# Kernel optimization log

Measured on AMD Instinct MI355X. Metric: run time of the kernel, lower is better.

The kernel has to match this reference:

```python
import jax, jax.numpy as jnp
import numpy as np

EPS = 1e-8


def _conv1d(x, w, b):
    # x: [B, E, L], w: [F, E, K], b: [F] -> [B, F, L] (k=3, pad=1 keeps length)
    y = jax.lax.conv_general_dilated(
        x, w, window_strides=(1,), padding=[(1, 1)],
        dimension_numbers=("NCH", "OIH", "NCH"))
    return y + b[None, :, None]


def setup_inputs() -> dict:
    key = jax.random.key(0)
    kq, ka, ke, kw, kb, ku = jax.random.split(key, 6)
    B, QL, AL = 512, 128, 512
    V, E, F, K = 50000, 300, 400, 3
    question = jax.random.randint(kq, (B, QL), 0, V + 1, dtype=jnp.int64)
    answer = jax.random.randint(ka, (B, AL), 0, V + 1, dtype=jnp.int64)
    emb_table = jax.random.normal(ke, (V + 1, E), dtype=jnp.float32)
    emb_table = emb_table.at[0].set(0.0)  # padding_idx=0
    conv_w = jax.random.normal(kw, (F, E, K), dtype=jnp.float32) * 0.05
    conv_b = jax.random.normal(kb, (F,), dtype=jnp.float32) * 0.05
    U = jax.random.normal(ku, (F, F), dtype=jnp.float32) * 0.1
    return {"question": question, "answer": answer, "emb_table": emb_table,
            "conv_w": conv_w, "conv_b": conv_b, "U": U}


def reference(question, answer, emb_table, conv_w, conv_b, U):
    q = emb_table[question]              # [B, QL, E]
    a = emb_table[answer]                # [B, AL, E]
    Q = _conv1d(q.transpose(0, 2, 1), conv_w, conv_b)   # [B, F, QL]
    A = _conv1d(a.transpose(0, 2, 1), conv_w, conv_b)   # [B, F, AL]
    # G = tanh(Q^T U A): [B, QL, AL]
    G = jnp.tanh(jnp.einsum("bfq,fg,bga->bqa", Q, U, A))
    roQ = jax.nn.softmax(jnp.max(G, axis=2), axis=1)    # [B, QL]
    roA = jax.nn.softmax(jnp.max(G, axis=1), axis=1)    # [B, AL]
    rQ = jnp.einsum("bfq,bq->bf", Q, roQ)               # [B, F]
    rA = jnp.einsum("bfa,ba->bf", A, roA)               # [B, F]
    nQ = jnp.maximum(jnp.linalg.norm(rQ, axis=1), EPS)
    nA = jnp.maximum(jnp.linalg.norm(rA, axis=1), EPS)
    return jnp.sum(rQ * rA, axis=1) / (nQ * nA)         # [B]
```

## Files before the change

### kernel.cpp

```cpp
#include <hip/hip_runtime.h>
#include <math.h>

typedef unsigned int   uint32;
typedef unsigned short ushort16;
typedef __attribute__((ext_vector_type(8))) short  short8;
typedef __attribute__((ext_vector_type(4))) float  floatx4;

#define Bb   512
#define QLn  128
#define ALn  512
#define En   300
#define Fn   400
#define OW   416
#define EPAD 320
#define NV   50001
#define ECROWS 50176
#define ECSTRIDE 2560

typedef const __attribute__((address_space(1))) unsigned int guint_t;
typedef __attribute__((address_space(3))) unsigned int luint_t;
#define GLDS16(g, l) __builtin_amdgcn_global_load_lds((guint_t*)(g), (luint_t*)(l), 16, 0, 0)

static __device__ __forceinline__ float bf_lo(uint32 u) { return __uint_as_float(u << 16); }
static __device__ __forceinline__ float bf_hi(uint32 u) { return __uint_as_float(u & 0xffff0000u); }
static __device__ __forceinline__ ushort16 f2bf(float f) {
    uint32 u = __float_as_uint(f);
    uint32 r = (u + 0x7fffu + ((u >> 16) & 1u)) >> 16;
    return (ushort16)r;
}
static __device__ __forceinline__ uint32 pack2(float a, float b) {
    return (uint32)f2bf(a) | ((uint32)f2bf(b) << 16);
}

__global__ __launch_bounds__(128) void embcvt_kernel(
        const float* __restrict__ emb, char* __restrict__ embbf)
{
    const int r = blockIdx.x, j = threadIdx.x;
    const float* er = emb + (size_t)r * En;
    uint32* orow = (uint32*)(embbf + (size_t)r * 640);
    for (int d = j; d < 160; d += 128) {
        uint32 v = 0;
        if (d < 150) {
            float2 f2v = *(const float2*)(er + 2 * d);
            v = pack2(f2v.x, f2v.y);
        }
        orow[d] = v;
    }
}

__global__ __launch_bounds__(256) void prep_wt(
        const float* __restrict__ W, const float* __restrict__ cb,
        ushort16* __restrict__ Wt2, float* __restrict__ bias2)
{
    const int f = blockIdx.x, t = threadIdx.x;
    for (int p2 = t; p2 < 480; p2 += 256) {
        int p = 2 * p2;
        float v0 = 0.f, v1 = 0.f;
        if (f < Fn) {
            int kk = p / EPAD, e = p - kk * EPAD;
            if (e < En)     v0 = W[(size_t)f * 900 + e * 3 + kk];
            if (e + 1 < En) v1 = W[(size_t)f * 900 + (e + 1) * 3 + kk];
        }
        *(uint32*)&Wt2[(size_t)f * 960 + p] = pack2(v0, v1);
    }
    if (t == 0) bias2[f] = (f < Fn) ? cb[f] : 0.f;
}

__global__ __launch_bounds__(256) void prep_ub(
        const float* __restrict__ U, ushort16* __restrict__ Ub)
{
    const int g = blockIdx.x, t = threadIdx.x;
    uint32* orow = (uint32*)(Ub + (size_t)g * 416);
    for (int f2 = t; f2 < 208; f2 += 256) {
        int f = 2 * f2;
        float v0 = 0.f, v1 = 0.f;
        if (g < Fn) {
            if (f < Fn)     v0 = U[(size_t)f * Fn + g];
            if (f + 1 < Fn) v1 = U[(size_t)(f + 1) * Fn + g];
        }
        orow[f2] = pack2(v0, v1);
    }
}

__global__ __launch_bounds__(512) void ec_gemm(
        const char* __restrict__ embbf, const char* __restrict__ Wt2,
        char* __restrict__ EC)
{
    __shared__ __align__(16) char As[32768];
    __shared__ __align__(16) char Bs[32768];
    const int t = threadIdx.x, lane = t & 63, w = t >> 6;
    const int v0 = blockIdx.x * 256, c0 = blockIdx.y * 256;
    const int wr = w >> 2, wc = w & 3;
    const int fm = lane & 15;
    const int cg = ((lane & 3) - ((lane >> 3) & 3)) & 3;
    const int rl = lane >> 2;
    const int chunkOff = (((lane >> 4) + (fm >> 1)) & 3) * 16;

    const char* srcA[2];
    const char* srcB[2];
#pragma unroll
    for (int i = 0; i < 2; ++i) {
        srcA[i] = embbf + (size_t)(v0 + w * 32 + i * 16 + rl) * 640 + cg * 16;
        int n = c0 + w * 32 + i * 16 + rl;
        int kk = n / 416, f = n - kk * 416;
        if (n >= 1248) { kk = 0; f = 508; }
        srcB[i] = Wt2 + (size_t)f * 1920 + kk * 640 + cg * 16;
    }
    char* AsW = As + w * 2048;
    char* BsW = Bs + w * 2048;

    floatx4 acc[8][4];
    const floatx4 zz = {0.f, 0.f, 0.f, 0.f};
#pragma unroll
    for (int m = 0; m < 8; ++m)
#pragma unroll
        for (int n = 0; n < 4; ++n) acc[m][n] = zz;

#define ESTG(ko, buf) do {                                                    \
        const int _ko = (ko); const int _bo = (buf) * 16384;                  \
        GLDS16(srcA[0] + _ko, AsW + _bo);                                     \
        GLDS16(srcA[1] + _ko, AsW + _bo + 1024);                              \
        GLDS16(srcB[0] + _ko, BsW + _bo);                                     \
        GLDS16(srcB[1] + _ko, BsW + _bo + 1024);                              \
    } while (0)

    int cur = 0;
    ESTG(0, 0);
    __syncthreads();
    for (int ks = 0; ks < 10; ++ks) {
        const int nxt = cur ^ 1;
        if (ks < 9) ESTG((ks + 1) * 64, nxt);
        short8 af[8], bfv[4];
        const char* Ac = As + cur * 16384;
        const char* Bc = Bs + cur * 16384;
#pragma unroll
        for (int m = 0; m < 8; ++m)
            af[m] = *(const short8*)(Ac + (wr * 128 + m * 16 + fm) * 64 + chunkOff);
#pragma unroll
        for (int n = 0; n < 4; ++n)
            bfv[n] = *(const short8*)(Bc + (wc * 64 + n * 16 + fm) * 64 + chunkOff);
        __builtin_amdgcn_s_setprio(1);
#pragma unroll
        for (int m = 0; m < 8; ++m)
#pragma unroll
            for (int n = 0; n < 4; ++n)
                acc[m][n] = __builtin_amdgcn_mfma_f32_16x16x32_bf16(
                    af[m], bfv[n], acc[m][n], 0, 0, 0);
        __builtin_amdgcn_s_setprio(0);
        __syncthreads();
        cur = nxt;
    }
#undef ESTG

#pragma unroll
    for (int m = 0; m < 8; ++m) {
        const int v = v0 + wr * 128 + m * 16 + ((lane >> 4) * 4);
#pragma unroll
        for (int n = 0; n < 4; ++n) {
            const int col = c0 + wc * 64 + n * 16 + fm;
#pragma unroll
            for (int r = 0; r < 4; ++r)
                *(ushort16*)(EC + (size_t)(v + r) * ECSTRIDE + col * 2) =
                    f2bf(acc[m][n][r]);
        }
    }
}

static __device__ __forceinline__ void gather_one(
        const int* __restrict__ toks, const char* __restrict__ EC,
        const float* __restrict__ bias2, char* __restrict__ outb,
        int id, int L)
{
    const uint32 uid = (uint32)id;
    const int c = (int)(uid % 52u);
    const int r = (int)(uid / 52u);
    const int l = r & (L - 1), b = r / L;
    const int* tr = toks + (size_t)b * L;
    const int t0 = (l > 0)     ? tr[l - 1] : 0;
    const int t1 = tr[l];
    const int t2 = (l < L - 1) ? tr[l + 1] : 0;
    const uint4 x0 = *(const uint4*)(EC + (size_t)t0 * ECSTRIDE +        c * 16);
    const uint4 x1 = *(const uint4*)(EC + (size_t)t1 * ECSTRIDE +  832 + c * 16);
    const uint4 x2 = *(const uint4*)(EC + (size_t)t2 * ECSTRIDE + 1664 + c * 16);
    const float4 b0 = *(const float4*)(bias2 + c * 8);
    const float4 b1 = *(const float4*)(bias2 + c * 8 + 4);
    uint4 o;
    o.x = pack2(bf_lo(x0.x) + bf_lo(x1.x) + bf_lo(x2.x) + b0.x,
                bf_hi(x0.x) + bf_hi(x1.x) + bf_hi(x2.x) + b0.y);
    o.y = pack2(bf_lo(x0.y) + bf_lo(x1.y) + bf_lo(x2.y) + b0.z,
                bf_hi(x0.y) + bf_hi(x1.y) + bf_hi(x2.y) + b0.w);
    o.z = pack2(bf_lo(x0.z) + bf_lo(x1.z) + bf_lo(x2.z) + b1.x,
                bf_hi(x0.z) + bf_hi(x1.z) + bf_hi(x2.z) + b1.y);
    o.w = pack2(bf_lo(x0.w) + bf_lo(x1.w) + bf_lo(x2.w) + b1.z,
                bf_hi(x0.w) + bf_hi(x1.w) + bf_hi(x2.w) + b1.w);
    *(uint4*)(outb + (size_t)r * 832 + c * 16) = o;
}

static __device__ __forceinline__ float red_sum_256(float v, volatile float* red) {
    int t = threadIdx.x;
    red[t] = v; __syncthreads();
    for (int s = 128; s > 0; s >>= 1) {
        if (t < s) red[t] = red[t] + red[t + s];
        __syncthreads();
    }
    float r = red[0]; __syncthreads();
    return r;
}

static __device__ __forceinline__ void pool_b_body(
        const float* __restrict__ scratch, float* __restrict__ out,
        int b, volatile float* red)
{
    const int t = threadIdx.x;
    float dd = 0.f, qq = 0.f, aam = 0.f;
    if (t < 208) {
        float q0 = 0.f, q1 = 0.f, a0 = 0.f, a1 = 0.f;
#pragma unroll
        for (int qtr = 0; qtr < 4; ++qtr) {
            const float* sc = scratch + ((size_t)b * 4 + qtr) * 832;
            q0 += sc[t]; q1 += sc[208 + t];
            a0 += sc[416 + t]; a1 += sc[624 + t];
        }
        dd  = q0 * a0 + q1 * a1;
        qq  = q0 * q0 + q1 * q1;
        aam = a0 * a0 + a1 * a1;
    }
    dd  = red_sum_256(dd, red);
    qq  = red_sum_256(qq, red);
    aam = red_sum_256(aam, red);
    if (t == 0) {
        float nq = fmaxf(sqrtf(qq), 1e-8f);
        float na = fmaxf(sqrtf(aam), 1e-8f);
        out[b] = dd / (nq * na);
    }
}

#define GQB 1024
#define GAB 4096
__global__ __launch_bounds__(256) void gather_both(
        const int* __restrict__ question, const int* __restrict__ answer,
        const char* __restrict__ EC, const float* __restrict__ bias2,
        char* __restrict__ qb, char* __restrict__ ab, int nb,
        const float* __restrict__ scrPrev, float* __restrict__ outPrev,
        int nbPrev)
{
    __shared__ float red[256];
    const int bx = blockIdx.x, t = threadIdx.x;
    if (bx < GQB) {
        const int total = nb * QLn * 52;
        for (int id = bx * 256 + t; id < total; id += GQB * 256)
            gather_one(question, EC, bias2, qb, id, QLn);
    } else if (bx < GQB + GAB) {
        const int total = nb * ALn * 52;
        for (int id = (bx - GQB) * 256 + t; id < total; id += GAB * 256)
            gather_one(answer, EC, bias2, ab, id, ALn);
    } else {
        const int b = bx - GQB - GAB;
        if (b < nbPrev) pool_b_body(scrPrev, outPrev, b, red);
    }
}

template<int MF, int NF, int BR>
static __device__ __forceinline__ void qp_tile64(
        const char* __restrict__ Qb, const char* __restrict__ Ub,
        char* __restrict__ ob, int col0, char* As, char* Bs)
{
    const int t = threadIdx.x, lane = t & 63, w = t >> 6;
    const int NWN = (MF == 4) ? 4 : 2;
    const int wr = w / NWN, wc = w % NWN;
    const int fm = lane & 15;
    const int cg = ((lane & 3) - ((lane >> 3) & 3)) & 3;
    const int rl = lane >> 2;
    const int chunkOff = (((lane >> 4) + (fm >> 1)) & 3) * 16;
    const int BUFB = BR * 64;

    const char* srcQ = Qb + (size_t)(w * 16 + rl) * 832 + cg * 16;
    const char* srcB0;
    const char* srcB1 = 0;
    if (BR == 256) {
        srcB0 = Ub + (size_t)(col0 + w * 64 + rl) * 832 + cg * 16;
    } else {
        srcB0 = Ub + (size_t)(col0 + w * 32 + rl) * 832 + cg * 16;
        srcB1 = Ub + (size_t)(col0 + 128 + w * 16 + rl) * 832 + cg * 16;
    }

    floatx4 acc[MF][NF];
    const floatx4 zz = {0.f, 0.f, 0.f, 0.f};
#pragma unroll
    for (int m = 0; m < MF; ++m)
#pragma unroll
        for (int n = 0; n < NF; ++n) acc[m][n] = zz;

#define QSTG(ko, buf) do {                                                    \
        const int _ko = (ko);                                                 \
        GLDS16(srcQ + _ko, As + (buf) * 4096 + w * 1024);                     \
        if (BR == 256) {                                                      \
            GLDS16(srcB0 + _ko,         Bs + (buf) * BUFB + w * 4096);        \
            GLDS16(srcB0 + 13312 + _ko, Bs + (buf) * BUFB + w * 4096 + 1024); \
            GLDS16(srcB0 + 26624 + _ko, Bs + (buf) * BUFB + w * 4096 + 2048); \
            GLDS16(srcB0 + 39936 + _ko, Bs + (buf) * BUFB + w * 4096 + 3072); \
        } else {                                                              \
            GLDS16(srcB0 + _ko,         Bs + (buf) * BUFB + w * 2048);        \
            GLDS16(srcB0 + 13312 + _ko, Bs + (buf) * BUFB + w * 2048 + 1024); \
            if (w < 2) GLDS16(srcB1 + _ko, Bs + (buf) * BUFB + 8192 + w * 1024); \
        }                                                                     \
    } while (0)

    int cur = 0;
    QSTG(0, 0);
    __syncthreads();
    for (int ks = 0; ks < 13; ++ks) {
        const int nxt = cur ^ 1;
        if (ks < 12) QSTG((ks + 1) * 64, nxt);
        short8 af[MF], bfv[NF];
        const char* Ac = As + cur * 4096;
        const char* Bc = Bs + cur * BUFB;
#pragma unroll
        for (int m = 0; m < MF; ++m)
            af[m] = *(const short8*)(Ac + (wr * (MF * 16) + m * 16 + fm) * 64 + chunkOff);
#pragma unroll
        for (int n = 0; n < NF; ++n)
            bfv[n] = *(const short8*)(Bc + (wc * (NF * 16) + n * 16 + fm) * 64 + chunkOff);
        __builtin_amdgcn_s_setprio(1);
#pragma unroll
        for (int m = 0; m < MF; ++m)
#pragma unroll
            for (int n = 0; n < NF; ++n)
                acc[m][n] = __builtin_amdgcn_mfma_f32_16x16x32_bf16(
                    af[m], bfv[n], acc[m][n], 0, 0, 0);
        __builtin_amdgcn_s_setprio(0);
        __syncthreads();
        cur = nxt;
    }
#undef QSTG

#pragma unroll
    for (int m = 0; m < MF; ++m) {
        const int row = wr * (MF * 16) + m * 16 + ((lane >> 4) * 4);
#pragma unroll
        for (int n = 0; n < NF; ++n) {
            const int col = col0 + wc * (NF * 16) + n * 16 + fm;
#pragma unroll
            for (int r = 0; r < 4; ++r)
                *(ushort16*)(ob + (size_t)(row + r) * 832 + col * 2) =
                    f2bf(acc[m][n][r]);
        }
    }
}

__global__ __launch_bounds__(256) void qp_gemm(
        const char* __restrict__ qb, const char* __restrict__ Ub,
        char* __restrict__ qpb, int nb)
{
    __shared__ __align__(16) char As[8192];
    __shared__ __align__(16) char Bs[32768];
    const int bx = blockIdx.x;
    const int xcd = bx & 7, rest = bx >> 3;
    const int nt = rest & 1, mh = (rest >> 1) & 1, b = (rest >> 2) * 8 + xcd;
    if (b >= nb) return;
    const char* Qb = qb + (size_t)b * 106496 + (size_t)mh * 64 * 832;
    char* ob = qpb + (size_t)b * 106496 + (size_t)mh * 64 * 832;
    if (nt == 0)
        qp_tile64<4, 4, 256>(Qb, Ub, ob, 0, As, Bs);
    else
        qp_tile64<2, 5, 160>(Qb, Ub, ob, 256, As, Bs);
}

__global__ __launch_bounds__(256) void fused_g(
        const ushort16* __restrict__ Qp,
        const ushort16* __restrict__ Av,
        float* __restrict__ rowPart,
        float* __restrict__ colMg,
        int nb)
{
    __shared__ __align__(16) char Qs[8192];
    __shared__ __align__(16) char Asl[32768];
    __shared__ float rowM4[64][4];

    const int t = threadIdx.x, lane = t & 63, w = t >> 6;
    const int bx = blockIdx.x;
    const int xcd = bx & 7, rest = bx >> 3;
    const int c = rest & 1, mh = (rest >> 1) & 1, b = (rest >> 2) * 8 + xcd;
    if (b >= nb) return;
    const int fm = lane & 15;
    const int cg = ((lane & 3) - ((lane >> 3) & 3)) & 3;
    const int rl = lane >> 2;
    const int chunkOff = (((lane >> 4) + (fm >> 1)) & 3) * 16;

    const char* Qpb = (const char*)Qp + (size_t)b * 106496 + (size_t)mh * 64 * 832;
    const char* Ab  = (const char*)Av + (size_t)b * 425984 + (size_t)c * 212992;
    const char* srcQ  = Qpb + (size_t)(w * 16 + rl) * 832 + cg * 16;
    const char* srcA0 = Ab  + (size_t)(w * 64 + rl) * 832 + cg * 16;

    floatx4 acc[4][4];
    const floatx4 zz = {0.f, 0.f, 0.f, 0.f};
#pragma unroll
    for (int m = 0; m < 4; ++m)
#pragma unroll
        for (int n = 0; n < 4; ++n) acc[m][n] = zz;

#define FSTG(ko, buf) do {                                                    \
        const int _ko = (ko);                                                 \
        GLDS16(srcQ + _ko,          Qs  + (buf) * 4096  + w * 1024);          \
        GLDS16(srcA0 + _ko,         Asl + (buf) * 16384 + w * 4096);          \
        GLDS16(srcA0 + 13312 + _ko, Asl + (buf) * 16384 + w * 4096 + 1024);   \
        GLDS16(srcA0 + 26624 + _ko, Asl + (buf) * 16384 + w * 4096 + 2048);   \
        GLDS16(srcA0 + 39936 + _ko, Asl + (buf) * 16384 + w * 4096 + 3072);   \
    } while (0)

    int cur = 0;
    FSTG(0, 0);
    __syncthreads();

    for (int ks = 0; ks < 13; ++ks) {
        const int nxt = cur ^ 1;
        if (ks < 12) FSTG((ks + 1) * 64, nxt);

        short8 qa[4], aa_[4];
        const char* Qc = Qs + cur * 4096;
        const char* Ac = Asl + cur * 16384;
#pragma unroll
        for (int m = 0; m < 4; ++m)
            qa[m] = *(const short8*)(Qc + (m * 16 + fm) * 64 + chunkOff);
#pragma unroll
        for (int n = 0; n < 4; ++n)
            aa_[n] = *(const short8*)(Ac + (w * 64 + n * 16 + fm) * 64 + chunkOff);
        __builtin_amdgcn_s_setprio(1);
#pragma unroll
        for (int m = 0; m < 4; ++m)
#pragma unroll
            for (int n = 0; n < 4; ++n)
                acc[m][n] = __builtin_amdgcn_mfma_f32_16x16x32_bf16(
                    qa[m], aa_[n], acc[m][n], 0, 0, 0);
        __builtin_amdgcn_s_setprio(0);
        __syncthreads();
        cur = nxt;
    }
#undef FSTG

#pragma unroll
    for (int m = 0; m < 4; ++m)
#pragma unroll
        for (int r = 0; r < 4; ++r) {
            float v = fmaxf(fmaxf(acc[m][0][r], acc[m][1][r]),
                            fmaxf(acc[m][2][r], acc[m][3][r]));
            v = fmaxf(v, __shfl_xor(v, 1));
            v = fmaxf(v, __shfl_xor(v, 2));
            v = fmaxf(v, __shfl_xor(v, 4));
            v = fmaxf(v, __shfl_xor(v, 8));
            if (fm == 0) rowM4[m * 16 + (lane >> 4) * 4 + r][w] = v;
        }
#pragma unroll
    for (int n = 0; n < 4; ++n) {
        float v = -1e30f;
#pragma unroll
        for (int m = 0; m < 4; ++m)
#pragma unroll
            for (int r = 0; r < 4; ++r) v = fmaxf(v, acc[m][n][r]);
        v = fmaxf(v, __shfl_xor(v, 16));
        v = fmaxf(v, __shfl_xor(v, 32));
        if (lane < 16)
            colMg[((size_t)b * 2 + mh) * 512 + c * 256 + w * 64 + n * 16 + lane] = v;
    }
    __syncthreads();
    if (t < 64)
        rowPart[((size_t)b * 2 + c) * 128 + mh * 64 + t] =
            fmaxf(fmaxf(rowM4[t][0], rowM4[t][1]),
                  fmaxf(rowM4[t][2], rowM4[t][3]));
}

static __device__ __forceinline__ float red_max_512(float v, volatile float* red) {
    int t = threadIdx.x;
    red[t] = v; __syncthreads();
    for (int s = 256; s > 0; s >>= 1) {
        if (t < s) red[t] = fmaxf(red[t], red[t + s]);
        __syncthreads();
    }
    float r = red[0]; __syncthreads();
    return r;
}
static __device__ __forceinline__ float red_sum_512(float v, volatile float* red) {
    int t = threadIdx.x;
    red[t] = v; __syncthreads();
    for (int s = 256; s > 0; s >>= 1) {
        if (t < s) red[t] = red[t] + red[t + s];
        __syncthreads();
    }
    float r = red[0]; __syncthreads();
    return r;
}

__global__ __launch_bounds__(512) void pool_a(
        const ushort16* __restrict__ Qv,
        const ushort16* __restrict__ Av,
        const float* __restrict__ rowPart,
        const float* __restrict__ colMg,
        float* __restrict__ scratch,
        int nb)
{
    __shared__ float colv[ALn];
    __shared__ float roq[QLn];
    __shared__ float red[512];
    __shared__ float part[2][4][208];
    const int t = threadIdx.x, bx = blockIdx.x;
    const int qtr = bx & 3, b = bx >> 2;

    float v = -1e30f;
    if (t < QLn) {
        const float* rp = rowPart + (size_t)b * 256;
        v = tanhf(fmaxf(rp[t], rp[128 + t]));
    }
    float vmax = red_max_512(v, red);
    float ex = (t < QLn) ? __expf(v - vmax) : 0.f;
    float ssum = red_sum_512(ex, red);
    if (t < QLn) roq[t] = ex / ssum;

    const float* cm = colMg + (size_t)b * 1024;
    float cv = tanhf(fmaxf(cm[t], cm[512 + t]));
    float cmax = red_max_512(cv, red);
    float e0 = __expf(cv - cmax);
    float csum = red_sum_512(e0, red);
    colv[t] = e0 / csum;
    __syncthreads();

    if (t < 416) {
        const int half = t / 208, c = t - half * 208;
        float rq0 = 0.f, rq1 = 0.f, ra0 = 0.f, ra1 = 0.f;
        const uint32* Qb32 = (const uint32*)((const char*)Qv + (size_t)b * 106496);
        const int q0r = qtr * 32 + half * 16;
#pragma unroll 4
        for (int q = q0r; q < q0r + 16; ++q) {
            float wv = roq[q];
            uint32 u = Qb32[q * 208 + c];
            rq0 = fmaf(bf_lo(u), wv, rq0);
            rq1 = fmaf(bf_hi(u), wv, rq1);
        }
        const uint32* Ab32 = (const uint32*)((const char*)Av + (size_t)b * 425984);
        const int a0r = qtr * 128 + half * 64;
#pragma unroll 4
        for (int a = a0r; a < a0r + 64; ++a) {
            float wv = colv[a];
            uint32 u = Ab32[a * 208 + c];
            ra0 = fmaf(bf_lo(u), wv, ra0);
            ra1 = fmaf(bf_hi(u), wv, ra1);
        }
        part[half][0][c] = rq0; part[half][1][c] = rq1;
        part[half][2][c] = ra0; part[half][3][c] = ra1;
    }
    __syncthreads();

    if (t < 208) {
        float* sc = scratch + ((size_t)b * 4 + qtr) * 832;
        sc[t]       = part[0][0][t] + part[1][0][t];
        sc[208 + t] = part[0][1][t] + part[1][1][t];
        sc[416 + t] = part[0][2][t] + part[1][2][t];
        sc[624 + t] = part[0][3][t] + part[1][3][t];
    }
}

__global__ __launch_bounds__(256) void pool_b(
        const float* __restrict__ scratch, float* __restrict__ out, int nb)
{
    __shared__ float red[256];
    pool_b_body(scratch, out, blockIdx.x, red);
}

extern "C" void kernel_launch(void* const* d_in, const int* in_sizes, int n_in,
                              void* d_out, int out_size, void* d_ws, size_t ws_size,
                              hipStream_t stream)
{
    const int*   question = (const int*)d_in[0];
    const int*   answer   = (const int*)d_in[1];
    const float* emb      = (const float*)d_in[2];
    const float* conv_w   = (const float*)d_in[3];
    const float* conv_b   = (const float*)d_in[4];
    const float* U        = (const float*)d_in[5];
    float* out = (float*)d_out;
    char* ws = (char*)d_ws;

    const size_t WT2B   = (size_t)512 * 960 * 2;
    const size_t UBB    = (size_t)416 * 416 * 2;
    const size_t ECB    = (size_t)ECROWS * ECSTRIDE;
    const size_t FIXED0 = WT2B + 2048 + UBB + ECB;
    const size_t QB     = (size_t)QLn * OW * 2;
    const size_t AB     = (size_t)ALn * OW * 2;
    const size_t MXB    = 20480;
    const size_t PER_B  = 2 * QB + AB + MXB;

    size_t avail = (ws_size > FIXED0) ? (ws_size - FIXED0) : 0;
    int CB = (int)(avail / PER_B);
    if (CB > Bb) CB = Bb;
    if (CB < 1)  CB = 1;
    int nch = (Bb + CB - 1) / CB;
    int CBe = (Bb + nch - 1) / nch;

    char*  wt2   = ws;
    float* bias2 = (float*)(ws + WT2B);
    char*  ub    = ws + WT2B + 2048;
    char*  EC    = ws + WT2B + 2048 + UBB;
    char*  embbf = ws + FIXED0;
    char*  qb    = ws + FIXED0;
    char*  qpb   = qb  + (size_t)CB * QB;
    char*  ab    = qpb + (size_t)CB * QB;
    float* rowP  = (float*)(ab + (size_t)CB * AB);
    float* colM  = rowP + (size_t)CB * 256;
    float* scr   = colM + (size_t)CB * 1024;

    embcvt_kernel<<<NV, 128, 0, stream>>>(emb, embbf);
    prep_wt<<<512, 256, 0, stream>>>(conv_w, conv_b, (ushort16*)wt2, bias2);
    prep_ub<<<416, 256, 0, stream>>>(U, (ushort16*)ub);
    ec_gemm<<<dim3(196, 5), 512, 0, stream>>>(embbf, wt2, EC);

    int prevNb = 0;
    float* prevOut = out;
    for (int b0 = 0; b0 < Bb; b0 += CBe) {
        int nb = (Bb - b0 < CBe) ? (Bb - b0) : CBe;
        int nb8 = (nb + 7) / 8;
        gather_both<<<GQB + GAB + prevNb, 256, 0, stream>>>(
            question + (size_t)b0 * QLn, answer + (size_t)b0 * ALn,
            EC, bias2, qb, ab, nb, scr, prevOut, prevNb);
        qp_gemm<<<nb8 * 32, 256, 0, stream>>>(qb, ub, qpb, nb);
        fused_g<<<nb8 * 32, 256, 0, stream>>>((const ushort16*)qpb, (const ushort16*)ab,
                                              rowP, colM, nb);
        pool_a<<<nb * 4, 512, 0, stream>>>((const ushort16*)qb, (const ushort16*)ab,
                                           rowP, colM, scr, nb);
        prevNb = nb;
        prevOut = out + b0;
    }
    pool_b<<<prevNb, 256, 0, stream>>>(scr, prevOut, prevNb);
}
```

Baseline: 559.1 us.

## Retile fused_g to full-Q by quarter-A tiles and split ec_gemm launch

The fused G kernel now has each block cover all 128 question rows against a quarter of the answer columns (an 8x2 MFMA tile per wave) instead of half-Q by half-A. This removes the split over the Q dimension, so column maxima come out complete and pool_a reads four row partials and one column value. The intent is a better MFMA-to-LDS-load ratio and fewer partial-max writes, at the cost of more Q reloads per A column. The ec_gemm launch is also split into two half-grid launches through a new base-offset parameter, which adds one launch.

Result: slower. 572.4 us (+2.4%).

```diff
diff --git a/kernel.cpp b/kernel.cpp
--- a/kernel.cpp
+++ b/kernel.cpp
@@ -84,12 +84,12 @@
 
 __global__ __launch_bounds__(512) void ec_gemm(
         const char* __restrict__ embbf, const char* __restrict__ Wt2,
-        char* __restrict__ EC)
+        char* __restrict__ EC, int vtBase)
 {
     __shared__ __align__(16) char As[32768];
     __shared__ __align__(16) char Bs[32768];
     const int t = threadIdx.x, lane = t & 63, w = t >> 6;
-    const int v0 = blockIdx.x * 256, c0 = blockIdx.y * 256;
+    const int v0 = (vtBase + blockIdx.x) * 256, c0 = blockIdx.y * 256;
     const int wr = w >> 2, wc = w & 3;
     const int fm = lane & 15;
     const int cg = ((lane & 3) - ((lane >> 3) & 3)) & 3;
@@ -373,39 +373,40 @@
         float* __restrict__ colMg,
         int nb)
 {
-    __shared__ __align__(16) char Qs[8192];
-    __shared__ __align__(16) char Asl[32768];
-    __shared__ float rowM4[64][4];
+    __shared__ __align__(16) char Qs[16384];
+    __shared__ __align__(16) char Asl[16384];
+    __shared__ float rowM4[128][4];
 
     const int t = threadIdx.x, lane = t & 63, w = t >> 6;
     const int bx = blockIdx.x;
     const int xcd = bx & 7, rest = bx >> 3;
-    const int c = rest & 1, mh = (rest >> 1) & 1, b = (rest >> 2) * 8 + xcd;
+    const int cq = rest & 3, b = (rest >> 2) * 8 + xcd;
     if (b >= nb) return;
     const int fm = lane & 15;
     const int cg = ((lane & 3) - ((lane >> 3) & 3)) & 3;
     const int rl = lane >> 2;
     const int chunkOff = (((lane >> 4) + (fm >> 1)) & 3) * 16;
 
-    const char* Qpb = (const char*)Qp + (size_t)b * 106496 + (size_t)mh * 64 * 832;
-    const char* Ab  = (const char*)Av + (size_t)b * 425984 + (size_t)c * 212992;
-    const char* srcQ  = Qpb + (size_t)(w * 16 + rl) * 832 + cg * 16;
-    const char* srcA0 = Ab  + (size_t)(w * 64 + rl) * 832 + cg * 16;
-
-    floatx4 acc[4][4];
+    const char* Qpb = (const char*)Qp + (size_t)b * 106496;
+    const char* Ab  = (const char*)Av + (size_t)b * 425984 + (size_t)cq * 128 * 832;
+    const char* srcQ0 = Qpb + (size_t)(w * 32 + rl) * 832 + cg * 16;
+    const char* srcQ1 = srcQ0 + (size_t)16 * 832;
+    const char* srcA0 = Ab + (size_t)(w * 32 + rl) * 832 + cg * 16;
+    const char* srcA1 = srcA0 + (size_t)16 * 832;
+
+    floatx4 acc[8][2];
     const floatx4 zz = {0.f, 0.f, 0.f, 0.f};
 #pragma unroll
-    for (int m = 0; m < 4; ++m)
-#pragma unroll
-        for (int n = 0; n < 4; ++n) acc[m][n] = zz;
+    for (int m = 0; m < 8; ++m)
+#pragma unroll
+        for (int n = 0; n < 2; ++n) acc[m][n] = zz;
 
 #define FSTG(ko, buf) do {                                                    \
         const int _ko = (ko);                                                 \
-        GLDS16(srcQ + _ko,          Qs  + (buf) * 4096  + w * 1024);          \
-        GLDS16(srcA0 + _ko,         Asl + (buf) * 16384 + w * 4096);          \
-        GLDS16(srcA0 + 13312 + _ko, Asl + (buf) * 16384 + w * 4096 + 1024);   \
-        GLDS16(srcA0 + 26624 + _ko, Asl + (buf) * 16384 + w * 4096 + 2048);   \
-        GLDS16(srcA0 + 39936 + _ko, Asl + (buf) * 16384 + w * 4096 + 3072);   \
+        GLDS16(srcQ0 + _ko, Qs  + (buf) * 8192 + w * 2048);                   \
+        GLDS16(srcQ1 + _ko, Qs  + (buf) * 8192 + w * 2048 + 1024);            \
+        GLDS16(srcA0 + _ko, Asl + (buf) * 8192 + w * 2048);                   \
+        GLDS16(srcA1 + _ko, Asl + (buf) * 8192 + w * 2048 + 1024);            \
     } while (0)
 
     int cur = 0;
@@ -416,20 +417,20 @@
         const int nxt = cur ^ 1;
         if (ks < 12) FSTG((ks + 1) * 64, nxt);
 
-        short8 qa[4], aa_[4];
-        const char* Qc = Qs + cur * 4096;
-        const char* Ac = Asl + cur * 16384;
-#pragma unroll
-        for (int m = 0; m < 4; ++m)
+        short8 qa[8], aa_[2];
+        const char* Qc = Qs + cur * 8192;
+        const char* Ac = Asl + cur * 8192;
+#pragma unroll
+        for (int m = 0; m < 8; ++m)
             qa[m] = *(const short8*)(Qc + (m * 16 + fm) * 64 + chunkOff);
 #pragma unroll
-        for (int n = 0; n < 4; ++n)
-            aa_[n] = *(const short8*)(Ac + (w * 64 + n * 16 + fm) * 64 + chunkOff);
+        for (int n = 0; n < 2; ++n)
+            aa_[n] = *(const short8*)(Ac + (w * 32 + n * 16 + fm) * 64 + chunkOff);
         __builtin_amdgcn_s_setprio(1);
 #pragma unroll
-        for (int m = 0; m < 4; ++m)
-#pragma unroll
-            for (int n = 0; n < 4; ++n)
+        for (int m = 0; m < 8; ++m)
+#pragma unroll
+            for (int n = 0; n < 2; ++n)
                 acc[m][n] = __builtin_amdgcn_mfma_f32_16x16x32_bf16(
                     qa[m], aa_[n], acc[m][n], 0, 0, 0);
         __builtin_amdgcn_s_setprio(0);
@@ -439,11 +440,10 @@
 #undef FSTG
 
 #pragma unroll
-    for (int m = 0; m < 4; ++m)
+    for (int m = 0; m < 8; ++m)
 #pragma unroll
         for (int r = 0; r < 4; ++r) {
-            float v = fmaxf(fmaxf(acc[m][0][r], acc[m][1][r]),
-                            fmaxf(acc[m][2][r], acc[m][3][r]));
+            float v = fmaxf(acc[m][0][r], acc[m][1][r]);
             v = fmaxf(v, __shfl_xor(v, 1));
             v = fmaxf(v, __shfl_xor(v, 2));
             v = fmaxf(v, __shfl_xor(v, 4));
@@ -451,20 +451,20 @@
             if (fm == 0) rowM4[m * 16 + (lane >> 4) * 4 + r][w] = v;
         }
 #pragma unroll
-    for (int n = 0; n < 4; ++n) {
+    for (int n = 0; n < 2; ++n) {
         float v = -1e30f;
 #pragma unroll
-        for (int m = 0; m < 4; ++m)
+        for (int m = 0; m < 8; ++m)
 #pragma unroll
             for (int r = 0; r < 4; ++r) v = fmaxf(v, acc[m][n][r]);
         v = fmaxf(v, __shfl_xor(v, 16));
         v = fmaxf(v, __shfl_xor(v, 32));
         if (lane < 16)
-            colMg[((size_t)b * 2 + mh) * 512 + c * 256 + w * 64 + n * 16 + lane] = v;
+            colMg[(size_t)b * 512 + cq * 128 + w * 32 + n * 16 + lane] = v;
     }
     __syncthreads();
-    if (t < 64)
-        rowPart[((size_t)b * 2 + c) * 128 + mh * 64 + t] =
+    if (t < 128)
+        rowPart[((size_t)b * 4 + cq) * 128 + t] =
             fmaxf(fmaxf(rowM4[t][0], rowM4[t][1]),
                   fmaxf(rowM4[t][2], rowM4[t][3]));
 }
@@ -507,16 +507,16 @@
 
     float v = -1e30f;
     if (t < QLn) {
-        const float* rp = rowPart + (size_t)b * 256;
-        v = tanhf(fmaxf(rp[t], rp[128 + t]));
+        const float* rp = rowPart + (size_t)b * 512;
+        v = tanhf(fmaxf(fmaxf(rp[t], rp[128 + t]),
+                        fmaxf(rp[256 + t], rp[384 + t])));
     }
     float vmax = red_max_512(v, red);
     float ex = (t < QLn) ? __expf(v - vmax) : 0.f;
     float ssum = red_sum_512(ex, red);
     if (t < QLn) roq[t] = ex / ssum;
 
-    const float* cm = colMg + (size_t)b * 1024;
-    float cv = tanhf(fmaxf(cm[t], cm[512 + t]));
+    float cv = tanhf(colMg[(size_t)b * 512 + t]);
     float cmax = red_max_512(cv, red);
     float e0 = __expf(cv - cmax);
     float csum = red_sum_512(e0, red);
@@ -603,13 +603,14 @@
     char*  qpb   = qb  + (size_t)CB * QB;
     char*  ab    = qpb + (size_t)CB * QB;
     float* rowP  = (float*)(ab + (size_t)CB * AB);
-    float* colM  = rowP + (size_t)CB * 256;
-    float* scr   = colM + (size_t)CB * 1024;
+    float* colM  = rowP + (size_t)CB * 512;
+    float* scr   = colM + (size_t)CB * 512;
 
     embcvt_kernel<<<NV, 128, 0, stream>>>(emb, embbf);
     prep_wt<<<512, 256, 0, stream>>>(conv_w, conv_b, (ushort16*)wt2, bias2);
     prep_ub<<<416, 256, 0, stream>>>(U, (ushort16*)ub);
-    ec_gemm<<<dim3(196, 5), 512, 0, stream>>>(embbf, wt2, EC);
+    ec_gemm<<<dim3(98, 5), 512, 0, stream>>>(embbf, wt2, EC, 0);
+    ec_gemm<<<dim3(98, 5), 512, 0, stream>>>(embbf, wt2, EC, 98);
 
     int prevNb = 0;
     float* prevOut = out;
```
